# Performance work log

Hardware: AMD Instinct MI355X
Metric: run time of the kernel (lower is better)

Reference implementation:

```python
import jax, jax.numpy as jnp
import numpy as np

D = 1024      # model_dim
H = 16        # num_heads
DH = D // H   # depth per head
F = 4096      # ffn_dim
B, L = 4, 2048
LN_EPS = 1e-5


def layer_norm(x, g, b):
    mu = jnp.mean(x, axis=-1, keepdims=True)
    var = jnp.var(x, axis=-1, keepdims=True)
    return (x - mu) * jax.lax.rsqrt(var + LN_EPS) * g + b


def setup_inputs() -> dict:
    key = jax.random.key(0)
    ks = jax.random.split(key, 12)
    s = 0.02
    return {
        "inputs": jax.random.normal(ks[0], (B, L, D), jnp.float32),
        "Wq": jax.random.normal(ks[1], (D, D), jnp.float32) * s,
        "Wk": jax.random.normal(ks[2], (D, D), jnp.float32) * s,
        "Wv": jax.random.normal(ks[3], (D, D), jnp.float32) * s,
        "Wo": jax.random.normal(ks[4], (D, D), jnp.float32) * s,
        "W1": jax.random.normal(ks[5], (F, D), jnp.float32) * s,
        "b1": jnp.zeros((F,), jnp.float32),
        "W2": jax.random.normal(ks[6], (D, F), jnp.float32) * s,
        "b2": jnp.zeros((D,), jnp.float32),
        "ln_g": jnp.ones((D,), jnp.float32),
        "ln_b": jnp.zeros((D,), jnp.float32),
    }


def reference(inputs, Wq, Wk, Wv, Wo, W1, b1, W2, b2, ln_g, ln_b):
    # --- MultiHeadAttention (faithful to source, incl. the bug where
    # ScaledDotProductAttention returns v, not attention @ v) ---
    scale = DH ** -0.5
    q = (inputs @ Wq.T) * scale            # [B,L,D], scaled before head split
    k = inputs @ Wk.T                      # [B,L,D]
    v = inputs @ Wv.T                      # [B,L,D]
    # only the LAST head's attention scores survive the python loop
    qH = q[..., (H - 1) * DH:]             # [B,L,DH]
    kH = k[..., (H - 1) * DH:]             # [B,L,DH]
    attn = jax.nn.softmax(jnp.einsum('bqd,bkd->bqk', qH, kH), axis=-1) / H
    # combine_heads(split_heads(v)) == v, so context = Wo applied to v
    context = v @ Wo.T                     # [B,L,D]; dropout(p=0) is identity

    # --- PositionalWiseFeedForward: conv1d(kernel=1) == pointwise linear ---
    h = jax.nn.relu(context @ W1.T + b1)   # [B,L,F]
    ffn = h @ W2.T + b2                    # [B,L,D]
    out = layer_norm(context + ffn, ln_g, ln_b)
    return out, attn
```

## Files before the change

### kernel.cpp

```cpp
#include <hip/hip_runtime.h>
#include <hip/hip_bf16.h>
#include <stdint.h>

#define D_ 1024
#define H_ 16
#define DH_ 64
#define F_ 4096
#define B_ 4
#define L_ 2048
#define MTOK 8192

typedef __attribute__((ext_vector_type(8))) short bf16x8;
typedef __attribute__((ext_vector_type(4))) float f32x4;

__device__ __forceinline__ short f2bf(float f) {
  uint32_t u = __float_as_uint(f);
  uint32_t r = (u + 0x7FFFu + ((u >> 16) & 1u)) >> 16;
  return (short)(uint16_t)r;
}
__device__ __forceinline__ float bf2f(short s) {
  return __uint_as_float(((uint32_t)(uint16_t)s) << 16);
}

__device__ __forceinline__ void gload_lds16(const short* g, short* l) {
  __builtin_amdgcn_global_load_lds(
      (const __attribute__((address_space(1))) void*)g,
      (__attribute__((address_space(3))) void*)l,
      16, 0, 0);
}

#define FENCE asm volatile("" ::: "memory")
#define BARX  do { FENCE; __builtin_amdgcn_s_barrier(); FENCE; } while (0)
#define PRIO1 __builtin_amdgcn_s_setprio(1)
#define PRIO0 __builtin_amdgcn_s_setprio(0)

__global__ void __launch_bounds__(256) convert_all(
    const float* __restrict__ Wq, const float* __restrict__ Wk,
    const float* __restrict__ Wv, const float* __restrict__ Wo,
    const float* __restrict__ W1, const float* __restrict__ W2,
    const float* __restrict__ inputs,
    short* __restrict__ wqk, short* __restrict__ wv, short* __restrict__ wo,
    short* __restrict__ w1, short* __restrict__ w2, short* __restrict__ in_bf) {
  long i = ((long)blockIdx.x * 256 + threadIdx.x) * 4;
  const float* src; short* dst; long off; float scale = 1.0f;
  if (i < 65536L)        { src = Wq + 960L * 1024; dst = wqk;         off = i;            scale = 0.125f; }
  else if (i < 131072L)  { src = Wk + 960L * 1024; dst = wqk + 65536; off = i - 65536L;   }
  else if (i < 1179648L) { src = Wv;     dst = wv;    off = i - 131072L;   }
  else if (i < 2228224L) { src = Wo;     dst = wo;    off = i - 1179648L;  }
  else if (i < 6422528L) { src = W1;     dst = w1;    off = i - 2228224L;  }
  else if (i < 10616832L){ src = W2;     dst = w2;    off = i - 6422528L;  }
  else                   { src = inputs; dst = in_bf; off = i - 10616832L; }
  float4 f = *(const float4*)(src + off);
  short4 o4;
  o4.x = f2bf(f.x * scale); o4.y = f2bf(f.y * scale);
  o4.z = f2bf(f.z * scale); o4.w = f2bf(f.w * scale);
  *(short4*)(dst + off) = o4;
}

__global__ void __launch_bounds__(256) transpose_bf16_1k(
    const short* __restrict__ src, short* __restrict__ dst) {
  __shared__ short t[64][65];
  const int bx = blockIdx.x, by = blockIdx.y;
  const int lr = threadIdx.x >> 4;
  const int lc = (threadIdx.x & 15) * 4;
#pragma unroll
  for (int rr = 0; rr < 4; rr++) {
    int r = lr * 4 + rr;
    short4 v = *(const short4*)&src[(long)(by * 64 + r) * 1024 + bx * 64 + lc];
    t[r][lc] = v.x; t[r][lc + 1] = v.y; t[r][lc + 2] = v.z; t[r][lc + 3] = v.w;
  }
  __syncthreads();
#pragma unroll
  for (int rr = 0; rr < 4; rr++) {
    int r = lr * 4 + rr;
    short4 v;
    v.x = t[lc + 0][r]; v.y = t[lc + 1][r];
    v.z = t[lc + 2][r]; v.w = t[lc + 3][r];
    *(short4*)&dst[(long)(bx * 64 + r) * 1024 + by * 64 + lc] = v;
  }
}


#define RD_A(mh_, par_) do {                                                  \
  const short* bp = lds + (par_) * BUF + wm * ASLOT;                          \
  _Pragma("unroll")                                                           \
  for (int m2 = 0; m2 < MH; m2++) {                                           \
    const int r = ((mh_) * MH + m2) * 16 + l15;                               \
    _Pragma("unroll")                                                         \
    for (int ks = 0; ks < 2; ks++)                                            \
      aF[mh_][m2][ks] =                                                       \
          *(const bf16x8*)(bp + r * 64 + (((ks * 4 + l4) ^ (r & 7)) << 3));   \
  } } while (0)

#define RD_B(nh_, par_) do {                                                  \
  const short* bp = lds + (par_) * BUF + BM * 64 + (wn >> 1) * 8192;          \
  _Pragma("unroll")                                                           \
  for (int n2 = 0; n2 < 2; n2++) {                                            \
    const int r = (wn & 1) * 64 + ((nh_) * 2 + n2) * 16 + l15;                \
    _Pragma("unroll")                                                         \
    for (int ks = 0; ks < 2; ks++)                                            \
      bF[nh_][n2][ks] =                                                       \
          *(const bf16x8*)(bp + r * 64 + (((ks * 4 + l4) ^ (r & 7)) << 3));   \
  } } while (0)

#define QUAD(mh_, nh_) do {                                                   \
  _Pragma("unroll")                                                           \
  for (int ks = 0; ks < 2; ks++)                                              \
    _Pragma("unroll")                                                         \
    for (int m2 = 0; m2 < MH; m2++)                                           \
      _Pragma("unroll")                                                       \
      for (int n2 = 0; n2 < 2; n2++)                                          \
        acc[(mh_) * MH + m2][(nh_) * 2 + n2] =                                \
            __builtin_amdgcn_mfma_f32_16x16x32_bf16(                          \
                aF[mh_][m2][ks], bF[nh_][n2][ks],                             \
                acc[(mh_) * MH + m2][(nh_) * 2 + n2], 0, 0, 0);               \
} while (0)

#define ITER2(g_, par_, SN, SPP, GK) do {                                     \
     \
  RD_B(0, par_); RD_A(0, par_); RD_B(1, par_);                                \
  if (SN) stA((g_) + 1, 1, (par_) ^ 1);                                       \
  PRIO1; QUAD(0, 0); QUAD(0, 1); PRIO0;                                       \
  BARX;           \
                                                                 \
  RD_A(1, par_);                                                              \
  if (SPP) { stB((g_) + 2, 0, par_); stB((g_) + 2, 1, par_);                  \
             stA((g_) + 2, 0, par_); }                                        \
  PRIO1; QUAD(1, 0); QUAD(1, 1); PRIO0;                                       \
  if (GK == 1) asm volatile("s_waitcnt vmcnt(%0)" :: "i"(VG) : "memory");     \
  else if (GK == 2) asm volatile("s_waitcnt vmcnt(0)" ::: "memory");          \
  BARX;                         \
} while (0)

template<int BMT, bool BIAS, bool RELU>
__global__ void __launch_bounds__(512, 2) gemm8p(
    const short* __restrict__ A, int lda,
    const short* __restrict__ Bm, int ldb,
    short* __restrict__ C, int ldc,
    const float* __restrict__ bias, int K) {
  constexpr int BM = BMT * 128;
  constexpr int MT = BMT * 4;
  constexpr int MH = MT / 2;
  constexpr int LA = BMT;
  constexpr int LB = 2;
  constexpr int ASLOT = (BM / 2) * 64;
  constexpr int BUF = BM * 64 + 16384;
  constexpr int VG = 2 * LB + LA;

  __shared__ __align__(16) short lds[2 * BUF];

  const int tid = threadIdx.x;
  const int lane = tid & 63;
  const int wave = tid >> 6;
  const int wm = wave >> 2, wn = wave & 3;
  const int l15 = lane & 15, l4 = lane >> 4;

  const int id = blockIdx.y * gridDim.x + blockIdx.x;
  const int per = (gridDim.x * gridDim.y) >> 3;
  const int swz = (id & 7) * per + (id >> 3);
  const int bn = swz % gridDim.x;
  const int bm = swz / gridDim.x;

  const short* Ab = A + (long)bm * BM * lda;
  const short* Bb = Bm + (long)bn * 256 * ldb;
  const int NTILE = K >> 6;

  const short* gA[2][LA]; short* dA[2][LA];
  const short* gB[2][LB]; short* dB[2][LB];
#pragma unroll
  for (int h = 0; h < 2; h++) {
#pragma unroll
    for (int l = 0; l < LA; l++) {
      int c = l * 512 + tid, r = c >> 3, cg = (c & 7) ^ (r & 7);
      gA[h][l] = Ab + (long)(h * (BM / 2) + r) * lda + cg * 8;
      dA[h][l] = lds + h * ASLOT + c * 8;
    }
#pragma unroll
    for (int l = 0; l < LB; l++) {
      int c = l * 512 + tid, r = c >> 3, cg = (c & 7) ^ (r & 7);
      gB[h][l] = Bb + (long)(h * 128 + r) * ldb + cg * 8;
      dB[h][l] = lds + BM * 64 + h * 8192 + c * 8;
    }
  }
  auto stA = [&](int t, int h, int par) {
#pragma unroll
    for (int l = 0; l < LA; l++)
      gload_lds16(gA[h][l] + (t << 6), dA[h][l] + par * BUF);
  };
  auto stB = [&](int t, int h, int par) {
#pragma unroll
    for (int l = 0; l < LB; l++)
      gload_lds16(gB[h][l] + (t << 6), dB[h][l] + par * BUF);
  };

  f32x4 acc[MT][4];
#pragma unroll
  for (int i = 0; i < MT; i++)
#pragma unroll
    for (int j = 0; j < 4; j++) acc[i][j] = (f32x4){0.f, 0.f, 0.f, 0.f};

  bf16x8 aF[2][MH][2];
  bf16x8 bF[2][2][2];

  stA(0, 0, 0); stA(0, 1, 0); stB(0, 0, 0); stB(0, 1, 0);
  stB(1, 0, 1); stB(1, 1, 1); stA(1, 0, 1);
  asm volatile("s_waitcnt vmcnt(%0)" :: "i"(VG) : "memory");
  BARX;

  for (int g = 0; g + 3 < NTILE; g += 2) {
    ITER2(g, 0, 1, 1, 1);
    ITER2(g + 1, 1, 1, 1, 1);
  }
  ITER2(NTILE - 2, 0, 1, 0, 2);
  ITER2(NTILE - 1, 1, 0, 0, 0);

  short* epi = lds + wave * 4608;
  const int col0 = bn * 256 + wn * 64;
  const int row0 = bm * BM + wm * (BM / 2);
  const int rg = lane >> 3, sg = lane & 7;
  float bb[4];
#pragma unroll
  for (int nt = 0; nt < 4; nt++)
    bb[nt] = BIAS ? bias[col0 + nt * 16 + l15] : 0.f;
#pragma unroll
  for (int h = 0; h < BMT; h++) {
#pragma unroll
    for (int m2 = 0; m2 < 4; m2++) {
#pragma unroll
      for (int nt = 0; nt < 4; nt++) {
#pragma unroll
        for (int r = 0; r < 4; r++) {
          float v = acc[h * 4 + m2][nt][r] + bb[nt];
          if (RELU) v = v > 0.f ? v : 0.f;
          epi[(m2 * 16 + l4 * 4 + r) * 72 + nt * 16 + l15] = f2bf(v);
        }
      }
    }
    FENCE;
#pragma unroll
    for (int it = 0; it < 8; it++) {
      const int rl = it * 8 + rg;
      bf16x8 vv = *(const bf16x8*)(epi + rl * 72 + sg * 8);
      *(bf16x8*)(C + (long)(row0 + h * 64 + rl) * ldc + col0 + sg * 8) = vv;
    }
    FENCE;
  }
}

__global__ void __launch_bounds__(256) gemm_bt(
    const short* __restrict__ A, int lda,
    const short* __restrict__ Bm, int ldb,
    short* __restrict__ C, int ldc, int K) {
  const int bn = blockIdx.x;
  const int bm = blockIdx.y;
  const short* Ab = A + (long)bm * 128 * lda;
  const short* Bb = Bm + (long)bn * 128 * ldb;

  __shared__ short lA[128 * 64];
  __shared__ short lB[128 * 64];

  const int tid = threadIdx.x;
  const int lane = tid & 63;
  const int wave = tid >> 6;
  const int wr = wave >> 1, wc = wave & 1;

  f32x4 acc[4][4];
#pragma unroll
  for (int i = 0; i < 4; i++)
#pragma unroll
    for (int j = 0; j < 4; j++) acc[i][j] = (f32x4){0.f, 0.f, 0.f, 0.f};

  for (int k0 = 0; k0 < K; k0 += 64) {
    __syncthreads();
#pragma unroll
    for (int i = 0; i < 4; i++) {
      int c = i * 256 + tid;
      int row = c >> 3;
      int col = (c & 7) * 8;
      gload_lds16(Ab + (long)row * lda + k0 + col, &lA[c * 8]);
      gload_lds16(Bb + (long)row * ldb + k0 + col, &lB[c * 8]);
    }
    __syncthreads();

#pragma unroll
    for (int ks = 0; ks < 2; ks++) {
      bf16x8 af[4], bfr[4];
#pragma unroll
      for (int t = 0; t < 4; t++) {
        af[t]  = *(const bf16x8*)&lA[(wr * 64 + t * 16 + (lane & 15)) * 64 + ks * 32 + (lane >> 4) * 8];
        bfr[t] = *(const bf16x8*)&lB[(wc * 64 + t * 16 + (lane & 15)) * 64 + ks * 32 + (lane >> 4) * 8];
      }
#pragma unroll
      for (int mt = 0; mt < 4; mt++)
#pragma unroll
        for (int nt = 0; nt < 4; nt++)
          acc[mt][nt] = __builtin_amdgcn_mfma_f32_16x16x32_bf16(af[mt], bfr[nt], acc[mt][nt], 0, 0, 0);
    }
  }

  const int col0 = bn * 128 + wc * 64;
  const int row0 = bm * 128 + wr * 64;
#pragma unroll
  for (int mt = 0; mt < 4; mt++) {
#pragma unroll
    for (int nt = 0; nt < 4; nt++) {
      int col = col0 + nt * 16 + (lane & 15);
      int rbase = row0 + mt * 16 + (lane >> 4) * 4;
#pragma unroll
      for (int r = 0; r < 4; r++)
        C[(long)(rbase + r) * ldc + col] = f2bf(acc[mt][nt][r]);
    }
  }
}

__global__ void __launch_bounds__(512) fused_attn(
    const short* __restrict__ qkh, float* __restrict__ attn) {
  const int tid = threadIdx.x;
  const int lane = tid & 63;
  const int wave = tid >> 6;
  const int l15 = lane & 15, l4 = lane >> 4;
  const int b = blockIdx.y;
  const int q0 = blockIdx.x * 16;
  const long base = (long)b * 2048;

  bf16x8 qf[2];
#pragma unroll
  for (int ks = 0; ks < 2; ks++)
    qf[ks] = *(const bf16x8*)&qkh[(base + q0 + l15) * 128 + ks * 32 + l4 * 8];

  const short* kb = qkh + (base + (long)wave * 256) * 128 + 64;

  f32x4 s[16];
#pragma unroll
  for (int kt = 0; kt < 16; kt++) {
    bf16x8 kf0 = *(const bf16x8*)&kb[(kt * 16 + l15) * 128 + l4 * 8];
    bf16x8 kf1 = *(const bf16x8*)&kb[(kt * 16 + l15) * 128 + 32 + l4 * 8];
    f32x4 a = (f32x4){0.f, 0.f, 0.f, 0.f};
    a = __builtin_amdgcn_mfma_f32_16x16x32_bf16(kf0, qf[0], a, 0, 0, 0);
    a = __builtin_amdgcn_mfma_f32_16x16x32_bf16(kf1, qf[1], a, 0, 0, 0);
    s[kt] = a;
  }

  float m = -1e30f;
#pragma unroll
  for (int kt = 0; kt < 16; kt++)
    m = fmaxf(m, fmaxf(fmaxf(s[kt][0], s[kt][1]), fmaxf(s[kt][2], s[kt][3])));
#pragma unroll
  for (int o = 16; o <= 32; o <<= 1) m = fmaxf(m, __shfl_xor(m, o, 64));

  float ss = 0.f;
#pragma unroll
  for (int kt = 0; kt < 16; kt++) {
    f32x4 e;
#pragma unroll
    for (int r = 0; r < 4; r++) e[r] = __expf(s[kt][r] - m);
    s[kt] = e;
    ss += (e[0] + e[1]) + (e[2] + e[3]);
  }
#pragma unroll
  for (int o = 16; o <= 32; o <<= 1) ss += __shfl_xor(ss, o, 64);

  __shared__ float lm[8][16], lsm[8][16];
  if (lane < 16) { lm[wave][l15] = m; lsm[wave][l15] = ss; }
  __syncthreads();
  float M = -1e30f;
#pragma unroll
  for (int w2 = 0; w2 < 8; w2++) M = fmaxf(M, lm[w2][l15]);
  float S = 0.f;
#pragma unroll
  for (int w2 = 0; w2 < 8; w2++) S += lsm[w2][l15] * __expf(lm[w2][l15] - M);
  const float f = __expf(m - M) / (S * 16.0f);

  float* attb = attn + (base + q0 + l15) * 2048 + wave * 256 + l4 * 4;
#pragma unroll
  for (int kt = 0; kt < 16; kt++) {
    f32x4 p;
#pragma unroll
    for (int r = 0; r < 4; r++) p[r] = s[kt][r] * f;
    *(f32x4*)(attb + kt * 16) = p;
  }
}

__device__ __forceinline__ float wave_sum(float v) {
#pragma unroll
  for (int o = 32; o > 0; o >>= 1) v += __shfl_xor(v, o, 64);
  return v;
}

__global__ void __launch_bounds__(256) ln_fuse(
    const short* __restrict__ ctx, const short* __restrict__ ffn,
    const float* __restrict__ g, const float* __restrict__ bta,
    float* __restrict__ out) {
  const int tid = threadIdx.x;
  long base = (long)blockIdx.x * 1024 + tid * 4;
  short4 c4 = *(const short4*)(ctx + base);
  short4 f4 = *(const short4*)(ffn + base);
  float x0 = bf2f(c4.x) + bf2f(f4.x);
  float x1 = bf2f(c4.y) + bf2f(f4.y);
  float x2 = bf2f(c4.z) + bf2f(f4.z);
  float x3 = bf2f(c4.w) + bf2f(f4.w);

  float s = (x0 + x1) + (x2 + x3);
  float q = (x0 * x0 + x1 * x1) + (x2 * x2 + x3 * x3);
  __shared__ float rs[4], rq[4];
  s = wave_sum(s);
  q = wave_sum(q);
  if ((tid & 63) == 0) { rs[tid >> 6] = s; rq[tid >> 6] = q; }
  __syncthreads();
  float S = rs[0] + rs[1] + rs[2] + rs[3];
  float Q = rq[0] + rq[1] + rq[2] + rq[3];
  float mu = S * (1.0f / 1024.0f);
  float var = Q * (1.0f / 1024.0f) - mu * mu;
  float inv = rsqrtf(var + 1e-5f);

  float4 g4 = *(const float4*)(g + tid * 4);
  float4 b4 = *(const float4*)(bta + tid * 4);
  float4 o;
  o.x = (x0 - mu) * inv * g4.x + b4.x;
  o.y = (x1 - mu) * inv * g4.y + b4.y;
  o.z = (x2 - mu) * inv * g4.z + b4.z;
  o.w = (x3 - mu) * inv * g4.w + b4.w;
  *(float4*)(out + base) = o;
}

extern "C" void kernel_launch(void* const* d_in, const int* in_sizes, int n_in,
                              void* d_out, int out_size, void* d_ws, size_t ws_size,
                              hipStream_t stream) {
  const float* inputs = (const float*)d_in[0];
  const float* Wq = (const float*)d_in[1];
  const float* Wk = (const float*)d_in[2];
  const float* Wv = (const float*)d_in[3];
  const float* Wo = (const float*)d_in[4];
  const float* W1 = (const float*)d_in[5];
  const float* b1 = (const float*)d_in[6];
  const float* W2 = (const float*)d_in[7];
  const float* b2 = (const float*)d_in[8];
  const float* ln_g = (const float*)d_in[9];
  const float* ln_b = (const float*)d_in[10];

  char* w = (char*)d_ws;
  short* in_bf = (short*)w;  w += (long)MTOK * D_ * 2;
  short* wqk   = (short*)w;  w += 128L * D_ * 2;
  short* wv    = (short*)w;  w += (long)D_ * D_ * 2;
  short* wo    = (short*)w;  w += (long)D_ * D_ * 2;
  short* w1    = (short*)w;  w += (long)F_ * D_ * 2;
  short* w2    = (short*)w;  w += (long)D_ * F_ * 2;
  short* qkh   = (short*)w;  w += (long)MTOK * 128 * 2;
  short* wvT   = (short*)w;  w += (long)D_ * D_ * 2;
  short* wf    = (short*)w;  w += (long)D_ * D_ * 2;
  short* ctxbf = (short*)w;  w += (long)MTOK * D_ * 2;
  short* hbf   = (short*)w;  w += (long)MTOK * F_ * 2;
  short* ffnbf = (short*)w;  w += (long)MTOK * D_ * 2;

  float* out  = (float*)d_out;
  float* attn = out + (long)MTOK * D_;

  convert_all<<<dim3(18560), 256, 0, stream>>>(
      Wq, Wk, Wv, Wo, W1, W2, inputs, wqk, wv, wo, w1, w2, in_bf);

  transpose_bf16_1k<<<dim3(16, 16), 256, 0, stream>>>(wv, wvT);
  gemm_bt<<<dim3(8, 8), 256, 0, stream>>>(wo, D_, wvT, D_, wf, D_, D_);

  gemm_bt<<<dim3(1, 64), 256, 0, stream>>>(in_bf, D_, wqk, D_, qkh, 128, D_);
  fused_attn<<<dim3(128, 4), 512, 0, stream>>>(qkh, attn);
  gemm8p<1, false, false><<<dim3(4, 64), 512, 0, stream>>>(
      in_bf, D_, wf, D_, ctxbf, D_, nullptr, D_);
  gemm8p<2, true, true><<<dim3(16, 32), 512, 0, stream>>>(
      ctxbf, D_, w1, D_, hbf, F_, b1, D_);
  gemm8p<1, true, false><<<dim3(4, 64), 512, 0, stream>>>(
      hbf, F_, w2, F_, ffnbf, D_, b2, F_);
  ln_fuse<<<dim3(MTOK), 256, 0, stream>>>(ctxbf, ffnbf, ln_g, ln_b, out);
}
```

Before: 263.5 us.

## Switch main GEMM to 32x32x16 MFMA and merge two small GEMM launches

The pipelined GEMM's inner product moves from 16x16x32 to 32x32x16 bf16 MFMA tiles, with new LDS fragment reads, accumulator layout and epilogue row mapping. Larger MFMA tiles reuse each fragment across more output and cut LDS reads per FLOP. Separately, the QK-head projection and the Wo*Wv weight fold now run as one 128-block launch, which saves one launch and lets both fill the GPU together. The new fragment-to-row mapping in the epilogue is a correctness risk.

```diff
diff --git a/kernel.cpp b/kernel.cpp
--- a/kernel.cpp
+++ b/kernel.cpp
@@ -12,6 +12,7 @@
 
 typedef __attribute__((ext_vector_type(8))) short bf16x8;
 typedef __attribute__((ext_vector_type(4))) float f32x4;
+typedef __attribute__((ext_vector_type(16))) float f32x16;
 
 __device__ __forceinline__ short f2bf(float f) {
   uint32_t u = __float_as_uint(f);
@@ -81,52 +82,51 @@
 }
 
 
-#define RD_A(mh_, par_) do {                                                  \
+#define RD_A32(mh_, par_) do {                                                \
   const short* bp = lds + (par_) * BUF + wm * ASLOT;                          \
   _Pragma("unroll")                                                           \
-  for (int m2 = 0; m2 < MH; m2++) {                                           \
-    const int r = ((mh_) * MH + m2) * 16 + l15;                               \
+  for (int m2 = 0; m2 < BMT; m2++) {                                          \
+    const int r = ((mh_) * BMT + m2) * 32 + l31;                              \
     _Pragma("unroll")                                                         \
-    for (int ks = 0; ks < 2; ks++)                                            \
+    for (int ks = 0; ks < 4; ks++) {                                          \
+      const int cg = ks * 2 + l32;                                            \
       aF[mh_][m2][ks] =                                                       \
-          *(const bf16x8*)(bp + r * 64 + (((ks * 4 + l4) ^ (r & 7)) << 3));   \
-  } } while (0)
-
-#define RD_B(nh_, par_) do {                                                  \
+          *(const bf16x8*)(bp + r * 64 + ((cg ^ (r & 7)) << 3));              \
+    } } } while (0)
+
+#define RD_B32(nh_, par_) do {                                                \
   const short* bp = lds + (par_) * BUF + BM * 64 + (wn >> 1) * 8192;          \
+  {                                                                           \
+    const int r = (wn & 1) * 64 + (nh_) * 32 + l31;                           \
+    _Pragma("unroll")                                                         \
+    for (int ks = 0; ks < 4; ks++) {                                          \
+      const int cg = ks * 2 + l32;                                            \
+      bF[nh_][ks] =                                                           \
+          *(const bf16x8*)(bp + r * 64 + ((cg ^ (r & 7)) << 3));              \
+    } } } while (0)
+
+#define QUAD32(mh_, nh_) do {                                                 \
   _Pragma("unroll")                                                           \
-  for (int n2 = 0; n2 < 2; n2++) {                                            \
-    const int r = (wn & 1) * 64 + ((nh_) * 2 + n2) * 16 + l15;                \
+  for (int ks = 0; ks < 4; ks++)                                              \
     _Pragma("unroll")                                                         \
-    for (int ks = 0; ks < 2; ks++)                                            \
-      bF[nh_][n2][ks] =                                                       \
-          *(const bf16x8*)(bp + r * 64 + (((ks * 4 + l4) ^ (r & 7)) << 3));   \
-  } } while (0)
-
-#define QUAD(mh_, nh_) do {                                                   \
-  _Pragma("unroll")                                                           \
-  for (int ks = 0; ks < 2; ks++)                                              \
-    _Pragma("unroll")                                                         \
-    for (int m2 = 0; m2 < MH; m2++)                                           \
-      _Pragma("unroll")                                                       \
-      for (int n2 = 0; n2 < 2; n2++)                                          \
-        acc[(mh_) * MH + m2][(nh_) * 2 + n2] =                                \
-            __builtin_amdgcn_mfma_f32_16x16x32_bf16(                          \
-                aF[mh_][m2][ks], bF[nh_][n2][ks],                             \
-                acc[(mh_) * MH + m2][(nh_) * 2 + n2], 0, 0, 0);               \
+    for (int m2 = 0; m2 < BMT; m2++)                                          \
+      acc[(mh_) * BMT + m2][nh_] =                                            \
+          __builtin_amdgcn_mfma_f32_32x32x16_bf16(                            \
+              aF[mh_][m2][ks], bF[nh_][ks],                                   \
+              acc[(mh_) * BMT + m2][nh_], 0, 0, 0);                           \
 } while (0)
 
 #define ITER2(g_, par_, SN, SPP, GK) do {                                     \
      \
-  RD_B(0, par_); RD_A(0, par_); RD_B(1, par_);                                \
+  RD_B32(0, par_); RD_A32(0, par_); RD_B32(1, par_);                          \
   if (SN) stA((g_) + 1, 1, (par_) ^ 1);                                       \
-  PRIO1; QUAD(0, 0); QUAD(0, 1); PRIO0;                                       \
+  PRIO1; QUAD32(0, 0); QUAD32(0, 1); PRIO0;                                   \
   BARX;           \
                                                                  \
-  RD_A(1, par_);                                                              \
+  RD_A32(1, par_);                                                            \
   if (SPP) { stB((g_) + 2, 0, par_); stB((g_) + 2, 1, par_);                  \
              stA((g_) + 2, 0, par_); }                                        \
-  PRIO1; QUAD(1, 0); QUAD(1, 1); PRIO0;                                       \
+  PRIO1; QUAD32(1, 0); QUAD32(1, 1); PRIO0;                                   \
   if (GK == 1) asm volatile("s_waitcnt vmcnt(%0)" :: "i"(VG) : "memory");     \
   else if (GK == 2) asm volatile("s_waitcnt vmcnt(0)" ::: "memory");          \
   BARX;                         \
@@ -139,8 +139,7 @@
     short* __restrict__ C, int ldc,
     const float* __restrict__ bias, int K) {
   constexpr int BM = BMT * 128;
-  constexpr int MT = BMT * 4;
-  constexpr int MH = MT / 2;
+  constexpr int MT2 = BMT * 2;
   constexpr int LA = BMT;
   constexpr int LB = 2;
   constexpr int ASLOT = (BM / 2) * 64;
@@ -153,7 +152,7 @@
   const int lane = tid & 63;
   const int wave = tid >> 6;
   const int wm = wave >> 2, wn = wave & 3;
-  const int l15 = lane & 15, l4 = lane >> 4;
+  const int l31 = lane & 31, l32 = lane >> 5;
 
   const int id = blockIdx.y * gridDim.x + blockIdx.x;
   const int per = (gridDim.x * gridDim.y) >> 3;
@@ -193,14 +192,16 @@
       gload_lds16(gB[h][l] + (t << 6), dB[h][l] + par * BUF);
   };
 
-  f32x4 acc[MT][4];
-#pragma unroll
-  for (int i = 0; i < MT; i++)
-#pragma unroll
-    for (int j = 0; j < 4; j++) acc[i][j] = (f32x4){0.f, 0.f, 0.f, 0.f};
-
-  bf16x8 aF[2][MH][2];
-  bf16x8 bF[2][2][2];
+  f32x16 acc[MT2][2];
+#pragma unroll
+  for (int i = 0; i < MT2; i++)
+#pragma unroll
+    for (int j = 0; j < 2; j++)
+#pragma unroll
+      for (int e = 0; e < 16; e++) acc[i][j][e] = 0.f;
+
+  bf16x8 aF[2][BMT][4];
+  bf16x8 bF[2][4];
 
   stA(0, 0, 0); stA(0, 1, 0); stB(0, 0, 0); stB(0, 1, 0);
   stB(1, 0, 1); stB(1, 1, 1); stA(1, 0, 1);
@@ -218,21 +219,23 @@
   const int col0 = bn * 256 + wn * 64;
   const int row0 = bm * BM + wm * (BM / 2);
   const int rg = lane >> 3, sg = lane & 7;
-  float bb[4];
-#pragma unroll
-  for (int nt = 0; nt < 4; nt++)
-    bb[nt] = BIAS ? bias[col0 + nt * 16 + l15] : 0.f;
+  float bb[2];
+#pragma unroll
+  for (int nf = 0; nf < 2; nf++)
+    bb[nf] = BIAS ? bias[col0 + nf * 32 + l31] : 0.f;
 #pragma unroll
   for (int h = 0; h < BMT; h++) {
 #pragma unroll
-    for (int m2 = 0; m2 < 4; m2++) {
-#pragma unroll
-      for (int nt = 0; nt < 4; nt++) {
-#pragma unroll
-        for (int r = 0; r < 4; r++) {
-          float v = acc[h * 4 + m2][nt][r] + bb[nt];
-          if (RELU) v = v > 0.f ? v : 0.f;
-          epi[(m2 * 16 + l4 * 4 + r) * 72 + nt * 16 + l15] = f2bf(v);
+    for (int m2 = 0; m2 < 2; m2++) {
+#pragma unroll
+      for (int nf = 0; nf < 2; nf++) {
+        f32x16 v = acc[h * 2 + m2][nf];
+#pragma unroll
+        for (int reg = 0; reg < 16; reg++) {
+          float x = v[reg] + bb[nf];
+          if (RELU) x = x > 0.f ? x : 0.f;
+          const int rl = m2 * 32 + (reg & 3) + 8 * (reg >> 2) + 4 * l32;
+          epi[rl * 72 + nf * 32 + l31] = f2bf(x);
         }
       }
     }
@@ -247,12 +250,18 @@
   }
 }
 
-__global__ void __launch_bounds__(256) gemm_bt(
-    const short* __restrict__ A, int lda,
-    const short* __restrict__ Bm, int ldb,
-    short* __restrict__ C, int ldc, int K) {
-  const int bn = blockIdx.x;
-  const int bm = blockIdx.y;
+__global__ void __launch_bounds__(256) gemm_small(
+    const short* __restrict__ in_bf, const short* __restrict__ wqk,
+    short* __restrict__ qkh,
+    const short* __restrict__ wo, const short* __restrict__ wvT,
+    short* __restrict__ wf) {
+  const short* A; const short* Bm; short* C;
+  int ldc, bn, bm;
+  const int bid = blockIdx.x;
+  if (bid < 64) { A = in_bf; Bm = wqk; C = qkh; ldc = 128; bn = 0; bm = bid; }
+  else { A = wo; Bm = wvT; C = wf; ldc = 1024; int b2 = bid - 64; bn = b2 & 7; bm = b2 >> 3; }
+  const int lda = 1024, ldb = 1024, K = 1024;
+
   const short* Ab = A + (long)bm * 128 * lda;
   const short* Bb = Bm + (long)bn * 128 * ldb;
 
@@ -459,9 +468,8 @@
       Wq, Wk, Wv, Wo, W1, W2, inputs, wqk, wv, wo, w1, w2, in_bf);
 
   transpose_bf16_1k<<<dim3(16, 16), 256, 0, stream>>>(wv, wvT);
-  gemm_bt<<<dim3(8, 8), 256, 0, stream>>>(wo, D_, wvT, D_, wf, D_, D_);
-
-  gemm_bt<<<dim3(1, 64), 256, 0, stream>>>(in_bf, D_, wqk, D_, qkh, 128, D_);
+  gemm_small<<<dim3(128), 256, 0, stream>>>(in_bf, wqk, qkh, wo, wvT, wf);
+
   fused_attn<<<dim3(128, 4), 512, 0, stream>>>(qkh, attn);
   gemm8p<1, false, false><<<dim3(4, 64), 512, 0, stream>>>(
       in_bf, D_, wf, D_, ctxbf, D_, nullptr, D_);
```

After: 281.8 us. +6.9%, slower.
